# Optimization experiments

Hardware: AMD Instinct MI355X
Metric: run time of the kernel (lower is better)

## Reference

```python
import jax, jax.numpy as jnp
import numpy as np

ALPHA = 0.9   # LIF membrane decay
VTH = 1.0     # LIF threshold
H = 8         # attention heads
ACH = 0.5     # acetylcholine level for thalamic gate

# Heaviside spike with fast-sigmoid surrogate gradient (standard SNN trick)
@jax.custom_vjp
def spike(v):
    return (v >= 0.0).astype(v.dtype)

def _spike_fwd(v):
    return (v >= 0.0).astype(v.dtype), v

def _spike_bwd(v, g):
    return (g / (1.0 + 2.0 * jnp.abs(v)) ** 2,)

spike.defvjp(_spike_fwd, _spike_bwd)

def lif(x):
    """Leaky-integrate-and-fire over time. x: (B,T,D) -> spikes (B,T,D). Soft reset."""
    def step(u, xt):
        u = ALPHA * u + xt
        s = spike(u - VTH)
        return u - s * VTH, s
    u0 = jnp.zeros_like(x[:, 0])
    _, s = jax.lax.scan(step, u0, jnp.swapaxes(x, 0, 1))  # scan over T
    return jnp.swapaxes(s, 0, 1)

def rwkv_wkv(k, v, w_decay, u_first):
    """Numerically-stable RWKV time-mixing recurrence. k,v: (B,T,D) -> wkv (B,T,D)."""
    w = jnp.exp(w_decay)  # positive per-channel decay
    def step(carry, kv):
        aa, bb, pp = carry
        kt, vt = kv
        ww = u_first + kt
        p = jnp.maximum(pp, ww)
        e1 = jnp.exp(pp - p); e2 = jnp.exp(ww - p)
        wkv = (e1 * aa + e2 * vt) / (e1 * bb + e2)
        ww2 = pp - w
        p2 = jnp.maximum(ww2, kt)
        e1 = jnp.exp(ww2 - p2); e2 = jnp.exp(kt - p2)
        return (e1 * aa + e2 * vt, e1 * bb + e2, p2), wkv
    B, T, D = k.shape
    init = (jnp.zeros((B, D), k.dtype), jnp.zeros((B, D), k.dtype),
            jnp.full((B, D), -1e30, k.dtype))
    _, wkv = jax.lax.scan(step, init, (jnp.swapaxes(k, 0, 1), jnp.swapaxes(v, 0, 1)))
    return jnp.swapaxes(wkv, 0, 1)


def setup_inputs() -> dict:
    key = jax.random.key(0)
    B, T, D = 4, 1024, 1024
    ks = jax.random.split(key, 16)
    s = 1.0 / np.sqrt(D)
    def W(k):
        return jax.random.normal(k, (D, D), jnp.float32) * s
    return {
        "x": jax.random.normal(ks[0], (B, T, D), jnp.float32),
        "context": jax.random.normal(ks[1], (B, T, D), jnp.float32),
        "Wg": W(ks[2]), "bg": jnp.zeros((D,), jnp.float32), "Wc": W(ks[3]),
        "Wq": W(ks[4]), "Wk": W(ks[5]), "Wv": W(ks[6]), "Wo": W(ks[7]),
        "Wm": W(ks[8]),
        "rWk": W(ks[9]), "rWv": W(ks[10]), "rWr": W(ks[11]), "rWo": W(ks[12]),
        "w_decay": jax.random.normal(ks[13], (D,), jnp.float32) * 0.1,
        "u_first": jax.random.normal(ks[14], (D,), jnp.float32) * 0.1,
        "gamma": jnp.ones((D,), jnp.float32), "beta": jnp.zeros((D,), jnp.float32),
    }


def reference(x, context, Wg, bg, Wc, Wq, Wk, Wv, Wo, Wm, rWk, rWv, rWr, rWo,
              w_decay, u_first, gamma, beta):
    B, T, D = x.shape
    dh = D // H
    # stage 1: thalamic gate (ach interpolates between pass-through and gated)
    gate = jax.nn.sigmoid(x @ Wg + bg + context @ Wc)
    gated = x * (ACH * gate + (1.0 - ACH))
    # stage 2: LIF integration (sequential over T)
    spikes2 = lif(gated)
    # stage 3: spike self-attention
    q = (spikes2 @ Wq).reshape(B, T, H, dh)
    k = (spikes2 @ Wk).reshape(B, T, H, dh)
    v = (spikes2 @ Wv).reshape(B, T, H, dh)
    scores = jnp.einsum('bthd,bshd->bhts', q, k) / np.sqrt(dh).astype(np.float32)
    attn = jax.nn.softmax(scores, axis=-1)
    attn_out = jnp.einsum('bhts,bshd->bthd', attn, v).reshape(B, T, D) @ Wo
    # stage 4: apical modulation by top-down context
    modulated = attn_out * (1.0 + jnp.tanh(context @ Wm))
    # stage 5: RWKV recurrence
    r = jax.nn.sigmoid(modulated @ rWr)
    wkv = rwkv_wkv(modulated @ rWk, modulated @ rWv, w_decay, u_first)
    recurrent = (r * wkv) @ rWo
    # stage 6: output LIF + residual + LayerNorm
    y = lif(recurrent) + spikes2
    mu = jnp.mean(y, axis=-1, keepdims=True)
    var = jnp.var(y, axis=-1, keepdims=True)
    return (y - mu) * jax.lax.rsqrt(var + 1e-5) * gamma + beta
```

## Files before the change

kernel.cpp:

```cpp
#include <hip/hip_runtime.h>
#include <hip/hip_bf16.h>
#include <math.h>

#define BDIM 4
#define TDIM 1024
#define DDIM 1024
#define DH   128
#define NELEM ((size_t)BDIM * TDIM * DDIM)

typedef __attribute__((ext_vector_type(8))) _Float16 hfrag;
typedef __attribute__((ext_vector_type(4))) float facc;

__device__ __forceinline__ void split2(float x, ushort& h1, ushort& h2) {
  const _Float16 a = (_Float16)x;
  const _Float16 b = (_Float16)((x - (float)a) * 2048.0f);
  union { _Float16 h; ushort u; } ua, ub;
  ua.h = a; ub.h = b;
  h1 = ua.u; h2 = ub.u;
}
#define INV2048 4.8828125e-4f

__device__ __forceinline__ float fexp(float x) {
  return __builtin_amdgcn_exp2f(x * 1.4426950408889634f);
}

constexpr int GM = 4096, GN = 1024, GK = 1024;
constexpr int BM = 128, BK = 32;
constexpr int BKP = 40;

__global__ __launch_bounds__(256)
void cvt_h2t(const float* __restrict__ W0, const float* __restrict__ W1,
             const float* __restrict__ W2, ushort* __restrict__ P,
             int zstride, int zkoff, int kTot) {
  __shared__ float Ls[64][68];
  const int z = blockIdx.z;
  const float* W = (z == 0) ? W0 : (z == 1 ? W1 : W2);
  ushort* Pz = P + (size_t)z * zstride;
  const size_t PS = (size_t)kTot * GN;
  const int t = threadIdx.x;
  const int k0 = blockIdx.x * 64, n0 = blockIdx.y * 64;
  const int r = t >> 4, c4 = (t & 15) << 2;
#pragma unroll
  for (int i = 0; i < 4; ++i)
    *(float4*)&Ls[r + i * 16][c4] =
        *(const float4*)(W + (size_t)(k0 + r + i * 16) * GN + n0 + c4);
  __syncthreads();
  const int n = t >> 2, kc = (t & 3) << 4;
  uint p1[8], p2[8];
#pragma unroll
  for (int jj = 0; jj < 8; ++jj) {
    const float x0 = Ls[kc + 2 * jj][n], x1 = Ls[kc + 2 * jj + 1][n];
    ushort a1, a2, b1, b2;
    split2(x0, a1, a2);
    split2(x1, b1, b2);
    p1[jj] = (uint)a1 | ((uint)b1 << 16);
    p2[jj] = (uint)a2 | ((uint)b2 << 16);
  }
  const int kk = k0 + kc + z * zkoff;
  ushort* d = Pz + (size_t)(kk >> 5) * (GN * 32) + (size_t)(n0 + n) * 32 + (kk & 31);
  *(uint4*)(d)          = *(uint4*)&p1[0];
  *(uint4*)(d + 8)      = *(uint4*)&p1[4];
  *(uint4*)(d + PS)     = *(uint4*)&p2[0];
  *(uint4*)(d + PS + 8) = *(uint4*)&p2[4];
}

template<int EPI, int AU8, int NMAT, int KTOT>
__global__ __launch_bounds__(256)
void gemm_k(const void* __restrict__ Av, const void* __restrict__ Av2,
            const ushort* __restrict__ pB,
            float* __restrict__ C0, float* __restrict__ C1,
            float* __restrict__ C2) {
  constexpr size_t PS = (size_t)KTOT * GN;
  __shared__ ushort As[2][BM][BKP];
  __shared__ ushort Bs[2][64][BKP];
  const int tid = threadIdx.x;
  const int n   = blockIdx.x;
  const int xcd = n & 7;
  const int idx = n >> 3;
  const int by  = xcd * 4 + (idx & 3);
  const int bx  = idx >> 2;
  const int mat = bx >> 4;
  const int row0 = by * BM;
  const int col0 = (bx & 15) * 64;
  const ushort* pBm = pB + (size_t)mat * 2 * PS;
  float* C = (mat == 0) ? C0 : (mat == 1 ? C1 : C2);

  const int sm  = tid & 127;
  const int sk0 = (tid >> 7) << 4;

  const int wave = tid >> 6;
  const int lane = tid & 63;
  const int wrow = (wave >> 1) * 64;
  const int wcol = (wave & 1) * 32;
  const int lrow = lane & 15;
  const int kof  = (lane >> 4) * 8;

  facc accM[4][2], accS[4][2];
#pragma unroll
  for (int i = 0; i < 4; ++i)
#pragma unroll
    for (int j = 0; j < 2; ++j) { accM[i][j] = (facc)0.f; accS[i][j] = (facc)0.f; }

  float av[16];
  uint4 a8raw;
  uint4 bregs[2];

  auto gloadA = [&](int K0) {
    const void* src = Av; int k = K0;
    if (KTOT > 1024 && K0 >= 1024) { src = Av2; k = K0 - 1024; }
    if (AU8) {
      a8raw = *(const uint4*)((const uint8_t*)src + (size_t)(row0 + sm) * 1024 + k + sk0);
    } else {
      const float* Ap = (const float*)src + (size_t)(row0 + sm) * 1024 + k + sk0;
      *(float4*)&av[0]  = *(const float4*)(Ap);
      *(float4*)&av[4]  = *(const float4*)(Ap + 4);
      *(float4*)&av[8]  = *(const float4*)(Ap + 8);
      *(float4*)&av[12] = *(const float4*)(Ap + 12);
    }
  };
  auto gloadB = [&](int K0) {
    const int kb = K0 >> 5;
#pragma unroll
    for (int j = 0; j < 2; ++j) {
      const int u = tid + 256 * j;
      const int q = u & 3, nn = (u >> 2) & 63, p = u >> 8;
      bregs[j] = *(const uint4*)(pBm + (size_t)p * PS + (size_t)kb * (GN * 32)
                                 + (size_t)(col0 + nn) * 32 + q * 8);
    }
  };
  auto swrite = [&]() {
    if (AU8) {
      const uint w4[4] = {a8raw.x, a8raw.y, a8raw.z, a8raw.w};
      uint pk[8];
#pragma unroll
      for (int i = 0; i < 8; ++i) {
        const uint b0 = (w4[i >> 1] >> ((i & 1) * 16)) & 0xFFu;
        const uint b1 = (w4[i >> 1] >> ((i & 1) * 16 + 8)) & 0xFFu;
        pk[i] = (b0 * 0x3C00u) | ((b1 * 0x3C00u) << 16);
      }
      *(uint4*)&As[0][sm][sk0]     = *(uint4*)&pk[0];
      *(uint4*)&As[0][sm][sk0 + 8] = *(uint4*)&pk[4];
    } else {
      uint q1[8], q2[8];
#pragma unroll
      for (int i = 0; i < 8; ++i) {
        ushort a1, a2, b1, b2;
        split2(av[2 * i], a1, a2);
        split2(av[2 * i + 1], b1, b2);
        q1[i] = (uint)a1 | ((uint)b1 << 16);
        q2[i] = (uint)a2 | ((uint)b2 << 16);
      }
      *(uint4*)&As[0][sm][sk0]     = *(uint4*)&q1[0];
      *(uint4*)&As[0][sm][sk0 + 8] = *(uint4*)&q1[4];
      *(uint4*)&As[1][sm][sk0]     = *(uint4*)&q2[0];
      *(uint4*)&As[1][sm][sk0 + 8] = *(uint4*)&q2[4];
    }
#pragma unroll
    for (int j = 0; j < 2; ++j) {
      const int u = tid + 256 * j;
      const int q = u & 3, nn = (u >> 2) & 63, p = u >> 8;
      *(uint4*)&Bs[p][nn][q * 8] = bregs[j];
    }
  };

  gloadA(0); gloadB(0);
  for (int k0 = 0; k0 < KTOT; k0 += BK) {
    __syncthreads();
    swrite();
    const int kn = k0 + BK;
    if (kn < KTOT) { gloadA(kn); gloadB(kn); }
    __syncthreads();
    hfrag fb1[2], fb2[2];
#pragma unroll
    for (int f = 0; f < 2; ++f) {
      fb1[f] = *(const hfrag*)&Bs[0][wcol + f * 16 + lrow][kof];
      fb2[f] = *(const hfrag*)&Bs[1][wcol + f * 16 + lrow][kof];
    }
#pragma unroll
    for (int mi = 0; mi < 4; ++mi) {
      const hfrag a1 = *(const hfrag*)&As[0][wrow + mi * 16 + lrow][kof];
      hfrag a2;
      if (!AU8) a2 = *(const hfrag*)&As[1][wrow + mi * 16 + lrow][kof];
#pragma unroll
      for (int ni = 0; ni < 2; ++ni)
        accM[mi][ni] = __builtin_amdgcn_mfma_f32_16x16x32_f16(a1, fb1[ni], accM[mi][ni], 0, 0, 0);
#pragma unroll
      for (int ni = 0; ni < 2; ++ni) {
        accS[mi][ni] = __builtin_amdgcn_mfma_f32_16x16x32_f16(a1, fb2[ni], accS[mi][ni], 0, 0, 0);
        if (!AU8)
          accS[mi][ni] = __builtin_amdgcn_mfma_f32_16x16x32_f16(a2, fb1[ni], accS[mi][ni], 0, 0, 0);
      }
    }
  }

#pragma unroll
  for (int mi = 0; mi < 4; ++mi) {
#pragma unroll
    for (int ni = 0; ni < 2; ++ni) {
      const int rbase = row0 + wrow + mi * 16 + (lane >> 4) * 4;
      const int cc    = col0 + wcol + ni * 16 + lrow;
      float* cp = C + (size_t)rbase * GN + cc;
#pragma unroll
      for (int r = 0; r < 4; ++r) {
        float v = accM[mi][ni][r] + accS[mi][ni][r] * INV2048;
        if (EPI == 1) v += cp[(size_t)r * GN];
        cp[(size_t)r * GN] = v;
      }
    }
  }
}

__device__ __forceinline__ float sigf(float z) { return 1.0f / (1.0f + expf(-z)); }

__global__ __launch_bounds__(256)
void gate_kernel(const float* __restrict__ x, const float* __restrict__ L,
                 const float* __restrict__ bg, float* __restrict__ out) {
  const int i4 = blockIdx.x * 256 + threadIdx.x;
  const float4 xv = ((const float4*)x)[i4];
  const float4 lv = ((const float4*)L)[i4];
  const float4 bv = ((const float4*)bg)[i4 & 255];
  float4 r;
  r.x = xv.x * (0.5f * sigf(lv.x + bv.x) + 0.5f);
  r.y = xv.y * (0.5f * sigf(lv.y + bv.y) + 0.5f);
  r.z = xv.z * (0.5f * sigf(lv.z + bv.z) + 0.5f);
  r.w = xv.w * (0.5f * sigf(lv.w + bv.w) + 0.5f);
  ((float4*)out)[i4] = r;
}

__global__ __launch_bounds__(256)
void mod_kernel(const float* __restrict__ a, const float* __restrict__ c,
                float* __restrict__ out) {
  const int i4 = blockIdx.x * 256 + threadIdx.x;
  const float4 av = ((const float4*)a)[i4];
  const float4 cv = ((const float4*)c)[i4];
  float4 r;
  r.x = av.x * (1.0f + tanhf(cv.x));
  r.y = av.y * (1.0f + tanhf(cv.y));
  r.z = av.z * (1.0f + tanhf(cv.z));
  r.w = av.w * (1.0f + tanhf(cv.w));
  ((float4*)out)[i4] = r;
}

__global__ __launch_bounds__(256)
void rmul_kernel(const float* __restrict__ rr, const float* __restrict__ wkv,
                 float* __restrict__ out) {
  const int i4 = blockIdx.x * 256 + threadIdx.x;
  const float4 rv = ((const float4*)rr)[i4];
  const float4 wv = ((const float4*)wkv)[i4];
  float4 r;
  r.x = sigf(rv.x) * wv.x;
  r.y = sigf(rv.y) * wv.y;
  r.z = sigf(rv.z) * wv.z;
  r.w = sigf(rv.w) * wv.w;
  ((float4*)out)[i4] = r;
}

__global__ __launch_bounds__(64)
void lif_u8_kernel(const float* __restrict__ x, uint8_t* __restrict__ s) {
  const int c = blockIdx.x * 64 + threadIdx.x;
  const size_t off = (size_t)(c >> 10) * TDIM * DDIM + (c & 1023);
  const float* xp = x + off;
  uint8_t* sp = s + off;
  float u = 0.f;
  float cur[16];
#pragma unroll
  for (int i = 0; i < 16; ++i) cur[i] = xp[(size_t)i * DDIM];
  for (int t = 0; t < TDIM; t += 16) {
    float nxt[16];
    if (t + 16 < TDIM) {
#pragma unroll
      for (int i = 0; i < 16; ++i) nxt[i] = xp[(size_t)(t + 16 + i) * DDIM];
    }
#pragma unroll
    for (int i = 0; i < 16; ++i) {
      u = __fadd_rn(__fmul_rn(0.9f, u), cur[i]);
      const bool fire = (u >= 1.0f);
      sp[(size_t)(t + i) * DDIM] = fire ? 1 : 0;
      if (fire) u -= 1.0f;
    }
#pragma unroll
    for (int i = 0; i < 16; ++i) cur[i] = nxt[i];
  }
}

__global__ __launch_bounds__(64)
void lif_ip_kernel(float* __restrict__ x) {
  const int c = blockIdx.x * 64 + threadIdx.x;
  const size_t off = (size_t)(c >> 10) * TDIM * DDIM + (c & 1023);
  float* xp = x + off;
  float u = 0.f;
  float cur[16];
#pragma unroll
  for (int i = 0; i < 16; ++i) cur[i] = xp[(size_t)i * DDIM];
  for (int t = 0; t < TDIM; t += 16) {
    float nxt[16];
    if (t + 16 < TDIM) {
#pragma unroll
      for (int i = 0; i < 16; ++i) nxt[i] = xp[(size_t)(t + 16 + i) * DDIM];
    }
#pragma unroll
    for (int i = 0; i < 16; ++i) {
      u = __fadd_rn(__fmul_rn(0.9f, u), cur[i]);
      const float sv = (u >= 1.0f) ? 1.0f : 0.0f;
      xp[(size_t)(t + i) * DDIM] = sv;
      u -= sv;
    }
#pragma unroll
    for (int i = 0; i < 16; ++i) cur[i] = nxt[i];
  }
}

__global__ __launch_bounds__(64)
void rwkv_kernel(const float* __restrict__ k, const float* __restrict__ v,
                 const float* __restrict__ wd, const float* __restrict__ uf,
                 float* __restrict__ out) {
  const int c = blockIdx.x * 64 + threadIdx.x;
  const int d = c & 1023;
  const size_t off = (size_t)(c >> 10) * TDIM * DDIM + d;
  const float* kp = k + off;
  const float* vp = v + off;
  float* op = out + off;
  const float w = expf(wd[d]);
  const float u = uf[d];
  float aa = 0.f, bb = 0.f, pp = -1e30f;
  float kc[8], vc[8];
#pragma unroll
  for (int i = 0; i < 8; ++i) {
    kc[i] = kp[(size_t)i * DDIM];
    vc[i] = vp[(size_t)i * DDIM];
  }
  for (int t = 0; t < TDIM; t += 8) {
    float kn[8], vn[8];
    if (t + 8 < TDIM) {
#pragma unroll
      for (int i = 0; i < 8; ++i) {
        kn[i] = kp[(size_t)(t + 8 + i) * DDIM];
        vn[i] = vp[(size_t)(t + 8 + i) * DDIM];
      }
    }
#pragma unroll
    for (int i = 0; i < 8; ++i) {
      const float kt = kc[i], vt = vc[i];
      const float ww = __fadd_rn(u, kt);
      const float p  = fmaxf(pp, ww);
      float e1 = fexp(__fsub_rn(pp, p));
      float e2 = fexp(__fsub_rn(ww, p));
      const float num = __fadd_rn(__fmul_rn(e1, aa), __fmul_rn(e2, vt));
      const float den = __fadd_rn(__fmul_rn(e1, bb), e2);
      op[(size_t)(t + i) * DDIM] = num * __builtin_amdgcn_rcpf(den);
      const float ww2 = __fsub_rn(pp, w);
      const float p2  = fmaxf(ww2, kt);
      e1 = fexp(__fsub_rn(ww2, p2));
      e2 = fexp(__fsub_rn(kt, p2));
      aa = __fadd_rn(__fmul_rn(e1, aa), __fmul_rn(e2, vt));
      bb = __fadd_rn(__fmul_rn(e1, bb), e2);
      pp = p2;
    }
#pragma unroll
    for (int i = 0; i < 8; ++i) { kc[i] = kn[i]; vc[i] = vn[i]; }
  }
}

__global__ __launch_bounds__(256)
void flash_attn(const float* __restrict__ Q, const float* __restrict__ K,
                const float* __restrict__ V, float* __restrict__ O) {
  __shared__ ushort Ks[2][32][136];
  __shared__ ushort Vt[2][128][40];
  __shared__ ushort Pl[4][2][16][40];
  const int tid = threadIdx.x;
  const int n    = blockIdx.x;
  const int xcd  = n & 7;
  const int idx  = n >> 3;
  const int qt   = idx & 15;
  const int grp4 = idx >> 4;
  const int p    = grp4 * 8 + xcd;
  const int b    = p >> 3, h = p & 7;
  const size_t base = ((size_t)b * TDIM) * DDIM + (size_t)h * DH;

  const int wave = tid >> 6;
  const int lane = tid & 63;
  const int lr   = lane & 15;
  const int g    = lane >> 4;
  const int sr   = tid >> 3;
  const int sc   = (tid & 7) * 16;
  const int vslot = (sr + 8 * (tid & 3)) & 31;

  hfrag q1[4], q2[4];
  {
    const float* Qrow = Q + base + (size_t)(qt * 64 + wave * 16 + lr) * DDIM;
#pragma unroll
    for (int s = 0; s < 4; ++s) {
      const float4 f0 = *(const float4*)(Qrow + s * 32 + g * 8);
      const float4 f1 = *(const float4*)(Qrow + s * 32 + g * 8 + 4);
      const float qf[8] = {f0.x, f0.y, f0.z, f0.w, f1.x, f1.y, f1.z, f1.w};
      union { hfrag v; ushort u[8]; } u1, u2;
#pragma unroll
      for (int j = 0; j < 8; ++j) split2(qf[j], u1.u[j], u2.u[j]);
      q1[s] = u1.v; q2[s] = u2.v;
    }
  }

  facc oM[8], oS[8];
#pragma unroll
  for (int i = 0; i < 8; ++i) { oM[i] = (facc)0.f; oS[i] = (facc)0.f; }
  float m[4] = {-INFINITY, -INFINITY, -INFINITY, -INFINITY};
  float l[4] = {0.f, 0.f, 0.f, 0.f};
  const float ISC = 0.08838834764831845f;

  float kv[16], vv[16];
  auto gload = [&](int kt0) {
    const float* Kg = K + base + (size_t)(kt0 + sr) * DDIM + sc;
    const float* Vg = V + base + (size_t)(kt0 + sr) * DDIM + sc;
    *(float4*)&kv[0]  = *(const float4*)(Kg);
    *(float4*)&kv[4]  = *(const float4*)(Kg + 4);
    *(float4*)&kv[8]  = *(const float4*)(Kg + 8);
    *(float4*)&kv[12] = *(const float4*)(Kg + 12);
    *(float4*)&vv[0]  = *(const float4*)(Vg);
    *(float4*)&vv[4]  = *(const float4*)(Vg + 4);
    *(float4*)&vv[8]  = *(const float4*)(Vg + 8);
    *(float4*)&vv[12] = *(const float4*)(Vg + 12);
  };
  gload(0);

  for (int kt0 = 0; kt0 < TDIM; kt0 += 32) {
    __syncthreads();
    {
      uint w1[8], w2[8];
#pragma unroll
      for (int i = 0; i < 8; ++i) {
        ushort a1, a2, b1, b2;
        split2(kv[2 * i], a1, a2);
        split2(kv[2 * i + 1], b1, b2);
        w1[i] = (uint)a1 | ((uint)b1 << 16);
        w2[i] = (uint)a2 | ((uint)b2 << 16);
      }
      *(uint4*)&Ks[0][sr][sc]     = *(uint4*)&w1[0];
      *(uint4*)&Ks[0][sr][sc + 8] = *(uint4*)&w1[4];
      *(uint4*)&Ks[1][sr][sc]     = *(uint4*)&w2[0];
      *(uint4*)&Ks[1][sr][sc + 8] = *(uint4*)&w2[4];
#pragma unroll
      for (int i = 0; i < 16; ++i) {
        ushort a1, a2;
        split2(vv[i], a1, a2);
        Vt[0][sc + i][vslot] = a1;
        Vt[1][sc + i][vslot] = a2;
      }
    }
    if (kt0 + 32 < TDIM) gload(kt0 + 32);
    __syncthreads();

    facc sM0 = (facc)0.f, sS0 = (facc)0.f, sM1 = (facc)0.f, sS1 = (facc)0.f;
#pragma unroll
    for (int s = 0; s < 4; ++s) {
      const int ko = s * 32 + g * 8;
      const hfrag kb10 = *(const hfrag*)&Ks[0][lr][ko];
      const hfrag kb11 = *(const hfrag*)&Ks[0][lr + 16][ko];
      const hfrag kb20 = *(const hfrag*)&Ks[1][lr][ko];
      const hfrag kb21 = *(const hfrag*)&Ks[1][lr + 16][ko];
      sM0 = __builtin_amdgcn_mfma_f32_16x16x32_f16(q1[s], kb10, sM0, 0, 0, 0);
      sS0 = __builtin_amdgcn_mfma_f32_16x16x32_f16(q1[s], kb20, sS0, 0, 0, 0);
      sS0 = __builtin_amdgcn_mfma_f32_16x16x32_f16(q2[s], kb10, sS0, 0, 0, 0);
      sM1 = __builtin_amdgcn_mfma_f32_16x16x32_f16(q1[s], kb11, sM1, 0, 0, 0);
      sS1 = __builtin_amdgcn_mfma_f32_16x16x32_f16(q1[s], kb21, sS1, 0, 0, 0);
      sS1 = __builtin_amdgcn_mfma_f32_16x16x32_f16(q2[s], kb11, sS1, 0, 0, 0);
    }

#pragma unroll
    for (int r = 0; r < 4; ++r) {
      const float sc0 = (sM0[r] + sS0[r] * INV2048) * ISC;
      const float sc1 = (sM1[r] + sS1[r] * INV2048) * ISC;
      float mx = fmaxf(sc0, sc1);
      mx = fmaxf(mx, __shfl_xor(mx, 1, 16));
      mx = fmaxf(mx, __shfl_xor(mx, 2, 16));
      mx = fmaxf(mx, __shfl_xor(mx, 4, 16));
      mx = fmaxf(mx, __shfl_xor(mx, 8, 16));
      const float mn = fmaxf(m[r], mx);
      const float rf = expf(m[r] - mn);
      const float p0 = expf(sc0 - mn), p1 = expf(sc1 - mn);
      float ps = p0 + p1;
      ps += __shfl_xor(ps, 1, 16);
      ps += __shfl_xor(ps, 2, 16);
      ps += __shfl_xor(ps, 4, 16);
      ps += __shfl_xor(ps, 8, 16);
      l[r] = l[r] * rf + ps;
      m[r] = mn;
#pragma unroll
      for (int nf = 0; nf < 8; ++nf) { oM[nf][r] *= rf; oS[nf][r] *= rf; }
      ushort a1, a2;
      split2(p0, a1, a2);
      Pl[wave][0][g * 4 + r][lr] = a1;
      Pl[wave][1][g * 4 + r][lr] = a2;
      split2(p1, a1, a2);
      Pl[wave][0][g * 4 + r][lr + 16] = a1;
      Pl[wave][1][g * 4 + r][lr + 16] = a2;
    }

    const hfrag pa1 = *(const hfrag*)&Pl[wave][0][lr][g * 8];
    const hfrag pa2 = *(const hfrag*)&Pl[wave][1][lr][g * 8];
#pragma unroll
    for (int nf = 0; nf < 8; ++nf) {
      const int vs = 8 * ((g + nf) & 3);
      const hfrag vb1 = *(const hfrag*)&Vt[0][nf * 16 + lr][vs];
      const hfrag vb2 = *(const hfrag*)&Vt[1][nf * 16 + lr][vs];
      oM[nf] = __builtin_amdgcn_mfma_f32_16x16x32_f16(pa1, vb1, oM[nf], 0, 0, 0);
      oS[nf] = __builtin_amdgcn_mfma_f32_16x16x32_f16(pa1, vb2, oS[nf], 0, 0, 0);
      oS[nf] = __builtin_amdgcn_mfma_f32_16x16x32_f16(pa2, vb1, oS[nf], 0, 0, 0);
    }
  }

  float* Og = O + base + (size_t)(qt * 64 + wave * 16) * DDIM;
#pragma unroll
  for (int r = 0; r < 4; ++r) {
    const float invl = 1.0f / l[r];
    float* orow = Og + (size_t)(g * 4 + r) * DDIM;
#pragma unroll
    for (int nf = 0; nf < 8; ++nf)
      orow[nf * 16 + lr] = (oM[nf][r] + oS[nf][r] * INV2048) * invl;
  }
}

__global__ __launch_bounds__(256)
void ln_kernel(const float* __restrict__ a, const uint8_t* __restrict__ s8,
               const float* __restrict__ gamma, const float* __restrict__ beta,
               float* __restrict__ out) {
  const int row = blockIdx.x;
  const int tid = threadIdx.x;
  const size_t base = (size_t)row * DDIM;
  const float4 av = *(const float4*)(a + base + tid * 4);
  const uchar4 sv = *(const uchar4*)(s8 + base + tid * 4);
  const float y0 = av.x + (float)sv.x, y1 = av.y + (float)sv.y;
  const float y2 = av.z + (float)sv.z, y3 = av.w + (float)sv.w;
  float s = (y0 + y1) + (y2 + y3);
  float q = (y0 * y0 + y1 * y1) + (y2 * y2 + y3 * y3);
#pragma unroll
  for (int off = 1; off < 64; off <<= 1) {
    s += __shfl_xor(s, off);
    q += __shfl_xor(q, off);
  }
  __shared__ float red[8];
  const int wid = tid >> 6;
  if ((tid & 63) == 0) { red[wid * 2] = s; red[wid * 2 + 1] = q; }
  __syncthreads();
  const float ts = (red[0] + red[2]) + (red[4] + red[6]);
  const float tq = (red[1] + red[3]) + (red[5] + red[7]);
  const float mu  = ts * (1.0f / 1024.0f);
  const float var = tq * (1.0f / 1024.0f) - mu * mu;
  const float rs  = 1.0f / sqrtf(var + 1e-5f);
  const int d = tid * 4;
  const float4 gv  = *(const float4*)(gamma + d);
  const float4 btv = *(const float4*)(beta + d);
  float4 r;
  r.x = (y0 - mu) * rs * gv.x + btv.x;
  r.y = (y1 - mu) * rs * gv.y + btv.y;
  r.z = (y2 - mu) * rs * gv.z + btv.z;
  r.w = (y3 - mu) * rs * gv.w + btv.w;
  *(float4*)(out + base + d) = r;
}

extern "C" void kernel_launch(void* const* d_in, const int* in_sizes, int n_in,
                              void* d_out, int out_size, void* d_ws, size_t ws_size,
                              hipStream_t stream) {
  const float* x       = (const float*)d_in[0];
  const float* context = (const float*)d_in[1];
  const float* Wg  = (const float*)d_in[2];
  const float* bg  = (const float*)d_in[3];
  const float* Wc  = (const float*)d_in[4];
  const float* Wq  = (const float*)d_in[5];
  const float* Wk  = (const float*)d_in[6];
  const float* Wv  = (const float*)d_in[7];
  const float* Wo  = (const float*)d_in[8];
  const float* Wm  = (const float*)d_in[9];
  const float* rWk = (const float*)d_in[10];
  const float* rWv = (const float*)d_in[11];
  const float* rWr = (const float*)d_in[12];
  const float* rWo = (const float*)d_in[13];
  const float* wd  = (const float*)d_in[14];
  const float* uf  = (const float*)d_in[15];
  const float* gamma = (const float*)d_in[16];
  const float* beta  = (const float*)d_in[17];
  float* out = (float*)d_out;

  float* w  = (float*)d_ws;
  float*   bA = w;
  float*   bC = w + 1 * NELEM;
  float*   bD = w + 2 * NELEM;
  uint8_t* bS = (uint8_t*)(w + 3 * NELEM);
  ushort*  pB = (ushort*)((uint8_t*)d_ws + 3 * NELEM * 4 + NELEM);

  const dim3 ew(4096);
  constexpr int M1 = 1024 * 1024;

  cvt_h2t<<<dim3(16, 16, 2), 256, 0, stream>>>(Wg, Wc, nullptr, pB, 0, 1024, 2048);
  gemm_k<0, 0, 1, 2048><<<512, 256, 0, stream>>>(x, context, pB, bA, nullptr, nullptr);
  gate_kernel<<<ew, 256, 0, stream>>>(x, bA, bg, bA);
  lif_u8_kernel<<<64, 64, 0, stream>>>(bA, bS);
  cvt_h2t<<<dim3(16, 16, 3), 256, 0, stream>>>(Wq, Wk, Wv, pB, 2 * M1, 0, 1024);
  gemm_k<0, 1, 3, 1024><<<1536, 256, 0, stream>>>(bS, nullptr, pB, bA, bC, bD);
  flash_attn<<<512, 256, 0, stream>>>(bA, bC, bD, bA);
  cvt_h2t<<<dim3(16, 16, 1), 256, 0, stream>>>(Wo, nullptr, nullptr, pB, 0, 0, 1024);
  gemm_k<0, 0, 1, 1024><<<512, 256, 0, stream>>>(bA, nullptr, pB, bC, nullptr, nullptr);
  cvt_h2t<<<dim3(16, 16, 1), 256, 0, stream>>>(Wm, nullptr, nullptr, pB, 0, 0, 1024);
  gemm_k<0, 0, 1, 1024><<<512, 256, 0, stream>>>(context, nullptr, pB, bA, nullptr, nullptr);
  mod_kernel<<<ew, 256, 0, stream>>>(bC, bA, bD);
  cvt_h2t<<<dim3(16, 16, 2), 256, 0, stream>>>(rWk, rWv, nullptr, pB, 2 * M1, 0, 1024);
  gemm_k<0, 0, 2, 1024><<<1024, 256, 0, stream>>>(bD, nullptr, pB, bA, bC, nullptr);
  rwkv_kernel<<<64, 64, 0, stream>>>(bA, bC, wd, uf, bA);
  cvt_h2t<<<dim3(16, 16, 1), 256, 0, stream>>>(rWr, nullptr, nullptr, pB, 0, 0, 1024);
  gemm_k<0, 0, 1, 1024><<<512, 256, 0, stream>>>(bD, nullptr, pB, bC, nullptr, nullptr);
  rmul_kernel<<<ew, 256, 0, stream>>>(bC, bA, bA);
  cvt_h2t<<<dim3(16, 16, 1), 256, 0, stream>>>(rWo, nullptr, nullptr, pB, 0, 0, 1024);
  gemm_k<0, 0, 1, 1024><<<512, 256, 0, stream>>>(bA, nullptr, pB, bC, nullptr, nullptr);
  lif_ip_kernel<<<64, 64, 0, stream>>>(bC);
  ln_kernel<<<4096, 256, 0, stream>>>(bC, bS, gamma, beta, out);
}
```

Measured before the change: 1.029 ms.

## Batch independent GEMMs with per-matrix A inputs, deepen prefetch in scans

The GEMM kernel now takes a separate A pointer per output matrix, so the Wo and Wm projections share one launch and rWk/rWv/rWr share another. This uses a new workspace buffer and removes several launches, along with the small-grid tail inefficiency of 512-block GEMMs. The LIF and RWKV sequential kernels double their register prefetch depth to hide more global-load latency, at the cost of more registers. The attention softmax switches expf to the hardware exp2-based fexp.

```diff
diff --git a/kernel.cpp b/kernel.cpp
--- a/kernel.cpp
+++ b/kernel.cpp
@@ -64,9 +64,10 @@
   *(uint4*)(d + PS + 8) = *(uint4*)&p2[4];
 }
 
-template<int EPI, int AU8, int NMAT, int KTOT>
+template<int EPI, int AU8, int KTOT>
 __global__ __launch_bounds__(256)
-void gemm_k(const void* __restrict__ Av, const void* __restrict__ Av2,
+void gemm_k(const void* __restrict__ A0, const void* __restrict__ A1,
+            const void* __restrict__ A2, const void* __restrict__ Ak2,
             const ushort* __restrict__ pB,
             float* __restrict__ C0, float* __restrict__ C1,
             float* __restrict__ C2) {
@@ -84,6 +85,7 @@
   const int col0 = (bx & 15) * 64;
   const ushort* pBm = pB + (size_t)mat * 2 * PS;
   float* C = (mat == 0) ? C0 : (mat == 1 ? C1 : C2);
+  const void* Abase = (mat == 0) ? A0 : (mat == 1 ? A1 : A2);
 
   const int sm  = tid & 127;
   const int sk0 = (tid >> 7) << 4;
@@ -106,8 +108,8 @@
   uint4 bregs[2];
 
   auto gloadA = [&](int K0) {
-    const void* src = Av; int k = K0;
-    if (KTOT > 1024 && K0 >= 1024) { src = Av2; k = K0 - 1024; }
+    const void* src = Abase; int k = K0;
+    if (KTOT > 1024 && K0 >= 1024) { src = Ak2; k = K0 - 1024; }
     if (AU8) {
       a8raw = *(const uint4*)((const uint8_t*)src + (size_t)(row0 + sm) * 1024 + k + sk0);
     } else {
@@ -262,24 +264,24 @@
   const float* xp = x + off;
   uint8_t* sp = s + off;
   float u = 0.f;
-  float cur[16];
-#pragma unroll
-  for (int i = 0; i < 16; ++i) cur[i] = xp[(size_t)i * DDIM];
-  for (int t = 0; t < TDIM; t += 16) {
-    float nxt[16];
-    if (t + 16 < TDIM) {
-#pragma unroll
-      for (int i = 0; i < 16; ++i) nxt[i] = xp[(size_t)(t + 16 + i) * DDIM];
-    }
-#pragma unroll
-    for (int i = 0; i < 16; ++i) {
+  float cur[32];
+#pragma unroll
+  for (int i = 0; i < 32; ++i) cur[i] = xp[(size_t)i * DDIM];
+  for (int t = 0; t < TDIM; t += 32) {
+    float nxt[32];
+    if (t + 32 < TDIM) {
+#pragma unroll
+      for (int i = 0; i < 32; ++i) nxt[i] = xp[(size_t)(t + 32 + i) * DDIM];
+    }
+#pragma unroll
+    for (int i = 0; i < 32; ++i) {
       u = __fadd_rn(__fmul_rn(0.9f, u), cur[i]);
       const bool fire = (u >= 1.0f);
       sp[(size_t)(t + i) * DDIM] = fire ? 1 : 0;
       if (fire) u -= 1.0f;
     }
 #pragma unroll
-    for (int i = 0; i < 16; ++i) cur[i] = nxt[i];
+    for (int i = 0; i < 32; ++i) cur[i] = nxt[i];
   }
 }
 
@@ -289,24 +291,24 @@
   const size_t off = (size_t)(c >> 10) * TDIM * DDIM + (c & 1023);
   float* xp = x + off;
   float u = 0.f;
-  float cur[16];
-#pragma unroll
-  for (int i = 0; i < 16; ++i) cur[i] = xp[(size_t)i * DDIM];
-  for (int t = 0; t < TDIM; t += 16) {
-    float nxt[16];
-    if (t + 16 < TDIM) {
-#pragma unroll
-      for (int i = 0; i < 16; ++i) nxt[i] = xp[(size_t)(t + 16 + i) * DDIM];
-    }
-#pragma unroll
-    for (int i = 0; i < 16; ++i) {
+  float cur[32];
+#pragma unroll
+  for (int i = 0; i < 32; ++i) cur[i] = xp[(size_t)i * DDIM];
+  for (int t = 0; t < TDIM; t += 32) {
+    float nxt[32];
+    if (t + 32 < TDIM) {
+#pragma unroll
+      for (int i = 0; i < 32; ++i) nxt[i] = xp[(size_t)(t + 32 + i) * DDIM];
+    }
+#pragma unroll
+    for (int i = 0; i < 32; ++i) {
       u = __fadd_rn(__fmul_rn(0.9f, u), cur[i]);
       const float sv = (u >= 1.0f) ? 1.0f : 0.0f;
       xp[(size_t)(t + i) * DDIM] = sv;
       u -= sv;
     }
 #pragma unroll
-    for (int i = 0; i < 16; ++i) cur[i] = nxt[i];
+    for (int i = 0; i < 32; ++i) cur[i] = nxt[i];
   }
 }
 
@@ -323,23 +325,23 @@
   const float w = expf(wd[d]);
   const float u = uf[d];
   float aa = 0.f, bb = 0.f, pp = -1e30f;
-  float kc[8], vc[8];
-#pragma unroll
-  for (int i = 0; i < 8; ++i) {
+  float kc[16], vc[16];
+#pragma unroll
+  for (int i = 0; i < 16; ++i) {
     kc[i] = kp[(size_t)i * DDIM];
     vc[i] = vp[(size_t)i * DDIM];
   }
-  for (int t = 0; t < TDIM; t += 8) {
-    float kn[8], vn[8];
-    if (t + 8 < TDIM) {
-#pragma unroll
-      for (int i = 0; i < 8; ++i) {
-        kn[i] = kp[(size_t)(t + 8 + i) * DDIM];
-        vn[i] = vp[(size_t)(t + 8 + i) * DDIM];
+  for (int t = 0; t < TDIM; t += 16) {
+    float kn[16], vn[16];
+    if (t + 16 < TDIM) {
+#pragma unroll
+      for (int i = 0; i < 16; ++i) {
+        kn[i] = kp[(size_t)(t + 16 + i) * DDIM];
+        vn[i] = vp[(size_t)(t + 16 + i) * DDIM];
       }
     }
 #pragma unroll
-    for (int i = 0; i < 8; ++i) {
+    for (int i = 0; i < 16; ++i) {
       const float kt = kc[i], vt = vc[i];
       const float ww = __fadd_rn(u, kt);
       const float p  = fmaxf(pp, ww);
@@ -357,7 +359,7 @@
       pp = p2;
     }
 #pragma unroll
-    for (int i = 0; i < 8; ++i) { kc[i] = kn[i]; vc[i] = vn[i]; }
+    for (int i = 0; i < 16; ++i) { kc[i] = kn[i]; vc[i] = vn[i]; }
   }
 }
 
@@ -475,8 +477,8 @@
       mx = fmaxf(mx, __shfl_xor(mx, 4, 16));
       mx = fmaxf(mx, __shfl_xor(mx, 8, 16));
       const float mn = fmaxf(m[r], mx);
-      const float rf = expf(m[r] - mn);
-      const float p0 = expf(sc0 - mn), p1 = expf(sc1 - mn);
+      const float rf = fexp(m[r] - mn);
+      const float p0 = fexp(sc0 - mn), p1 = fexp(sc1 - mn);
       float ps = p0 + p1;
       ps += __shfl_xor(ps, 1, 16);
       ps += __shfl_xor(ps, 2, 16);
@@ -584,32 +586,32 @@
   float*   bA = w;
   float*   bC = w + 1 * NELEM;
   float*   bD = w + 2 * NELEM;
-  uint8_t* bS = (uint8_t*)(w + 3 * NELEM);
-  ushort*  pB = (ushort*)((uint8_t*)d_ws + 3 * NELEM * 4 + NELEM);
+  float*   bE = w + 3 * NELEM;
+  uint8_t* bS = (uint8_t*)(w + 4 * NELEM);
+  ushort*  pB = (ushort*)((uint8_t*)d_ws + 4 * NELEM * 4 + NELEM);
 
   const dim3 ew(4096);
   constexpr int M1 = 1024 * 1024;
 
   cvt_h2t<<<dim3(16, 16, 2), 256, 0, stream>>>(Wg, Wc, nullptr, pB, 0, 1024, 2048);
-  gemm_k<0, 0, 1, 2048><<<512, 256, 0, stream>>>(x, context, pB, bA, nullptr, nullptr);
+  gemm_k<0, 0, 2048><<<512, 256, 0, stream>>>(x, nullptr, nullptr, context, pB,
+                                              bA, nullptr, nullptr);
   gate_kernel<<<ew, 256, 0, stream>>>(x, bA, bg, bA);
   lif_u8_kernel<<<64, 64, 0, stream>>>(bA, bS);
   cvt_h2t<<<dim3(16, 16, 3), 256, 0, stream>>>(Wq, Wk, Wv, pB, 2 * M1, 0, 1024);
-  gemm_k<0, 1, 3, 1024><<<1536, 256, 0, stream>>>(bS, nullptr, pB, bA, bC, bD);
+  gemm_k<0, 1, 1024><<<1536, 256, 0, stream>>>(bS, bS, bS, nullptr, pB, bA, bC, bD);
   flash_attn<<<512, 256, 0, stream>>>(bA, bC, bD, bA);
-  cvt_h2t<<<dim3(16, 16, 1), 256, 0, stream>>>(Wo, nullptr, nullptr, pB, 0, 0, 1024);
-  gemm_k<0, 0, 1, 1024><<<512, 256, 0, stream>>>(bA, nullptr, pB, bC, nullptr, nullptr);
-  cvt_h2t<<<dim3(16, 16, 1), 256, 0, stream>>>(Wm, nullptr, nullptr, pB, 0, 0, 1024);
-  gemm_k<0, 0, 1, 1024><<<512, 256, 0, stream>>>(context, nullptr, pB, bA, nullptr, nullptr);
-  mod_kernel<<<ew, 256, 0, stream>>>(bC, bA, bD);
-  cvt_h2t<<<dim3(16, 16, 2), 256, 0, stream>>>(rWk, rWv, nullptr, pB, 2 * M1, 0, 1024);
-  gemm_k<0, 0, 2, 1024><<<1024, 256, 0, stream>>>(bD, nullptr, pB, bA, bC, nullptr);
+  cvt_h2t<<<dim3(16, 16, 2), 256, 0, stream>>>(Wo, Wm, nullptr, pB, 2 * M1, 0, 1024);
+  gemm_k<0, 0, 1024><<<1024, 256, 0, stream>>>(bA, context, nullptr, nullptr, pB,
+                                               bC, bE, nullptr);
+  mod_kernel<<<ew, 256, 0, stream>>>(bC, bE, bD);
+  cvt_h2t<<<dim3(16, 16, 3), 256, 0, stream>>>(rWk, rWv, rWr, pB, 2 * M1, 0, 1024);
+  gemm_k<0, 0, 1024><<<1536, 256, 0, stream>>>(bD, bD, bD, nullptr, pB, bA, bC, bE);
   rwkv_kernel<<<64, 64, 0, stream>>>(bA, bC, wd, uf, bA);
-  cvt_h2t<<<dim3(16, 16, 1), 256, 0, stream>>>(rWr, nullptr, nullptr, pB, 0, 0, 1024);
-  gemm_k<0, 0, 1, 1024><<<512, 256, 0, stream>>>(bD, nullptr, pB, bC, nullptr, nullptr);
-  rmul_kernel<<<ew, 256, 0, stream>>>(bC, bA, bA);
+  rmul_kernel<<<ew, 256, 0, stream>>>(bE, bA, bA);
   cvt_h2t<<<dim3(16, 16, 1), 256, 0, stream>>>(rWo, nullptr, nullptr, pB, 0, 0, 1024);
-  gemm_k<0, 0, 1, 1024><<<512, 256, 0, stream>>>(bA, nullptr, pB, bC, nullptr, nullptr);
+  gemm_k<0, 0, 1024><<<512, 256, 0, stream>>>(bA, nullptr, nullptr, nullptr, pB,
+                                              bC, nullptr, nullptr);
   lif_ip_kernel<<<64, 64, 0, stream>>>(bC);
   ln_kernel<<<4096, 256, 0, stream>>>(bC, bS, gamma, beta, out);
 }
```

Result: faster. 972.1 us (-5.5%).
